# Optimization experiments

Measured on AMD Instinct MI355X. Metric: run time of the kernel, lower is better.

## Reference

```python
import jax, jax.numpy as jnp
import numpy as np

NDIM, NINEQ, NEQ = 1024, 512, 256
EPS = 1e-4       # Q regularization (module's eps)
N_ITERS = 25     # fixed primal-dual interior-point iterations
SIGMA = 0.1      # centering parameter


def setup_inputs() -> dict:
    key = jax.random.key(0)
    ks = jax.random.split(key, 5)
    L = jnp.tril(jax.random.uniform(ks[0], (NDIM, NDIM)))                      # tril(rand) as in torch init
    q = jax.random.uniform(ks[1], (NDIM,), minval=-1.0, maxval=1.0)
    G = jax.random.uniform(ks[2], (NINEQ, NDIM), minval=-1.0, maxval=1.0)
    A = jax.random.uniform(ks[3], (NEQ, NDIM), minval=-1.0, maxval=1.0)
    b = jax.random.uniform(ks[4], (NEQ,), minval=-1.0, maxval=1.0)
    x0 = jnp.zeros((NDIM,), jnp.float32)   # nn.Parameter(torch.zeros(ndim))
    s0 = jnp.ones((NINEQ,), jnp.float32)   # nn.Parameter(torch.ones(nineq))
    return {"L": L, "q": q, "G": G, "A": A, "b": b, "x0": x0, "s0": s0}


def _frac_to_boundary(v, dv):
    # max step alpha in (0,1] keeping v + alpha*dv > 0, with 0.99 backoff
    safe_dv = jnp.where(dv < 0, dv, -1.0)
    ratio = jnp.where(dv < 0, -v / safe_dv, 1.0)
    return jnp.min(ratio)


def _solve_qp(Q, q, G, h, A, b):
    n, m, p = q.shape[0], h.shape[0], b.shape[0]

    def step(state, _):
        x, s, z, y = state
        r_x = Q @ x + q + G.T @ z + A.T @ y          # dual residual
        r_p = G @ x + s - h                           # primal ineq residual
        r_y = A @ x - b                               # primal eq residual
        mu = jnp.dot(s, z) / m
        r_c = s * z - SIGMA * mu                      # centered complementarity
        D = z / s                                     # diag scaling
        H = Q + G.T @ (D[:, None] * G)                # reduced Hessian [n,n]
        KKT = jnp.block([[H, A.T], [A, jnp.zeros((p, p), Q.dtype)]])
        rhs = jnp.concatenate([-(r_x + G.T @ ((-r_c + z * r_p) / s)), -r_y])
        sol = jnp.linalg.solve(KKT, rhs)
        dx, dy = sol[:n], sol[n:]
        ds = -r_p - G @ dx
        dz = (-r_c - z * ds) / s
        alpha = 0.99 * jnp.minimum(1.0, jnp.minimum(_frac_to_boundary(s, ds), _frac_to_boundary(z, dz)))
        return (x + alpha * dx, s + alpha * ds, z + alpha * dz, y + alpha * dy), None

    init = (jnp.zeros((n,), Q.dtype), jnp.ones((m,), Q.dtype), jnp.ones((m,), Q.dtype), jnp.zeros((p,), Q.dtype))
    (x, s, z, y), _ = jax.lax.scan(step, init, None, length=N_ITERS)
    return x


def reference(L, q, G, A, b, x0, s0):
    Lt = jnp.tril(L)  # M * L with M = tril(ones)
    Q = Lt @ Lt.T + EPS * jnp.eye(L.shape[0], dtype=L.dtype)
    h = G @ x0 + s0   # learn_h branch (source's self.z0 is self.x0)
    return _solve_qp(Q, q, G, h, A, b)
```

## Files before the change

kernel.cpp:

```cpp
#include <hip/hip_runtime.h>
#include <hip/hip_bf16.h>


constexpr int ND = 1024;
constexpr int MI = 512;
constexpr int PE = 256;
constexpr int NM = 512;
constexpr int LDM = 520;
constexpr double EPSQ = 1e-4;
constexpr double SIG = 0.1;
constexpr int NITER = 25;

__device__ __forceinline__ double wred(double v) {
#pragma unroll
  for (int off = 32; off; off >>= 1) v += __shfl_down(v, off, 64);
  return v;
}

__global__ void k_prep(const float* __restrict__ Gf, const float* __restrict__ Af,
                       const float* __restrict__ qf, const float* __restrict__ bf,
                       float* __restrict__ GTf, float* __restrict__ ATf,
                       double* __restrict__ qd, double* __restrict__ bd,
                       double* __restrict__ xv, double* __restrict__ sv,
                       double* __restrict__ zv, double* __restrict__ yv,
                       double* __restrict__ scal) {
  if (blockIdx.x == 0 && threadIdx.x == 0) { scal[0] = 1.0; scal[1] = 0.0; }
  for (size_t idx = (size_t)blockIdx.x * blockDim.x + threadIdx.x;
       idx < (size_t)MI * ND; idx += (size_t)gridDim.x * blockDim.x) {
    int k = (int)(idx >> 10), i = (int)(idx & 1023);
    GTf[(size_t)i * MI + k] = Gf[idx];
    if (idx < (size_t)PE * ND) ATf[(size_t)i * PE + k] = Af[idx];
    if (idx < ND) { qd[idx] = (double)qf[idx]; xv[idx] = 0.0; }
    if (idx < MI) { sv[idx] = 1.0; zv[idx] = 1.0; }
    if (idx < PE) { bd[idx] = (double)bf[idx]; yv[idx] = 0.0; }
  }
}

__global__ __launch_bounds__(256) void k_h(const float* __restrict__ Gf,
                                           const float* __restrict__ x0f,
                                           const float* __restrict__ s0f,
                                           double* __restrict__ hd) {
  int wid = blockIdx.x * 4 + (int)(threadIdx.x >> 6), lane = threadIdx.x & 63;
  if (wid >= MI) return;
  double acc = 0;
  for (int c = lane; c < ND; c += 64) acc += (double)Gf[(size_t)wid * ND + c] * (double)x0f[c];
  acc = wred(acc);
  if (lane == 0) hd[wid] = acc + (double)s0f[wid];
}

__global__ __launch_bounds__(256) void k_qbuild(const float* __restrict__ Lf,
                                                double* __restrict__ Qd, double* __restrict__ LQ) {
  __shared__ double As[32][33], Bs[32][33];
  int i0 = blockIdx.y * 32, j0 = blockIdx.x * 32;
  int tx = threadIdx.x & 15, ty = threadIdx.x >> 4;
  double acc[2][2] = {};
  int kmax = (i0 < j0 ? i0 : j0) + 32;
  for (int k0 = 0; k0 < kmax; k0 += 32) {
    for (int l = threadIdx.x; l < 1024; l += 256) {
      int r = l >> 5, c = l & 31;
      As[r][c] = (k0 + c <= i0 + r) ? (double)Lf[(size_t)(i0 + r) * ND + k0 + c] : 0.0;
      Bs[r][c] = (k0 + c <= j0 + r) ? (double)Lf[(size_t)(j0 + r) * ND + k0 + c] : 0.0;
    }
    __syncthreads();
#pragma unroll
    for (int k = 0; k < 32; k++) {
      double a0 = As[2 * ty][k], a1 = As[2 * ty + 1][k];
      double b0 = Bs[2 * tx][k], b1 = Bs[2 * tx + 1][k];
      acc[0][0] += a0 * b0; acc[0][1] += a0 * b1;
      acc[1][0] += a1 * b0; acc[1][1] += a1 * b1;
    }
    __syncthreads();
  }
  for (int da = 0; da < 2; da++)
    for (int db = 0; db < 2; db++) {
      int i = i0 + 2 * ty + da, j = j0 + 2 * tx + db;
      double v = acc[da][db] + (i == j ? EPSQ : 0.0);
      Qd[(size_t)i * ND + j] = v;
      LQ[(size_t)i * ND + j] = v;
    }
}

__global__ __launch_bounds__(256) void k_chol_diag_inv(double* __restrict__ A, int lda, int kb,
                                                       double* __restrict__ DG) {
  __shared__ double a[64][65];
  __shared__ double invp[2080];
  __shared__ double dfloor;
  int t = threadIdx.x;
  size_t base = (size_t)kb * 64;
  for (int l = t; l < 4096; l += 256) { int r = l >> 6, c = l & 63; a[r][c] = A[(base + r) * lda + base + c]; }
  __syncthreads();
  if (t == 0) {
    double m = 0;
    for (int i = 0; i < 64; i++) m = fmax(m, fabs(a[i][i]));
    dfloor = m * 1e-28 + 1e-280;
  }
  __syncthreads();
  for (int j = 0; j < 64; j++) {
    if (t == 0) a[j][j] = sqrt(fmax(a[j][j], dfloor));
    __syncthreads();
    double piv = a[j][j];
    for (int r = j + 1 + t; r < 64; r += 256) a[r][j] /= piv;
    __syncthreads();
    int w = 63 - j;
    for (int l = t; l < w * w; l += 256) {
      int rr = j + 1 + l / w, cc = j + 1 + l % w;
      if (cc <= rr) a[rr][cc] -= a[rr][j] * a[cc][j];
    }
    __syncthreads();
  }
  for (int l = t; l < 4096; l += 256) { int r = l >> 6, c = l & 63; if (c <= r) A[(base + r) * lda + base + c] = a[r][c]; }
  if (t < 64) {
    int c = t;
    for (int i = c; i < 64; i++) {
      double v = (i == c) ? 1.0 : 0.0;
      for (int k = c; k < i; k++) v -= a[i][k] * invp[k * (k + 1) / 2 + c];
      invp[i * (i + 1) / 2 + c] = v / a[i][i];
    }
  }
  __syncthreads();
  for (int l = t; l < 4096; l += 256) {
    int r = l >> 6, c = l & 63;
    DG[(size_t)kb * 4096 + (size_t)c * 64 + r] = (c <= r) ? invp[r * (r + 1) / 2 + c] : 0.0;
  }
}

__global__ __launch_bounds__(256) void k_diag2(double* __restrict__ A, int lda, int kb,
                                               double* __restrict__ DG) {
  __shared__ double sh[6400];
  int t = threadIdx.x;
  if (blockIdx.x == 0) {
    double* a = sh;
    double* invp = sh + 4160;
    size_t base = (size_t)kb * 64;
    for (int l = t; l < 4096; l += 256) { int r = l >> 6, c = l & 63; a[r * 65 + c] = A[(base + r) * lda + base + c]; }
    __syncthreads();
    if (t == 0) {
      double m = 0;
      for (int i = 0; i < 64; i++) m = fmax(m, fabs(a[i * 65 + i]));
      sh[6272] = m * 1e-28 + 1e-280;
    }
    __syncthreads();
    double dfloor = sh[6272];
    for (int j = 0; j < 64; j++) {
      if (t == 0) a[j * 65 + j] = sqrt(fmax(a[j * 65 + j], dfloor));
      __syncthreads();
      double piv = a[j * 65 + j];
      for (int r = j + 1 + t; r < 64; r += 256) a[r * 65 + j] /= piv;
      __syncthreads();
      int w = 63 - j;
      for (int l = t; l < w * w; l += 256) {
        int rr = j + 1 + l / w, cc = j + 1 + l % w;
        if (cc <= rr) a[rr * 65 + cc] -= a[rr * 65 + j] * a[cc * 65 + j];
      }
      __syncthreads();
    }
    for (int l = t; l < 4096; l += 256) { int r = l >> 6, c = l & 63; if (c <= r) A[(base + r) * lda + base + c] = a[r * 65 + c]; }
    if (t < 64) {
      int c = t;
      for (int i = c; i < 64; i++) {
        double v = (i == c) ? 1.0 : 0.0;
        for (int k = c; k < i; k++) v -= a[i * 65 + k] * invp[k * (k + 1) / 2 + c];
        invp[i * (i + 1) / 2 + c] = v / a[i * 65 + i];
      }
    }
    __syncthreads();
    for (int l = t; l < 4096; l += 256) {
      int r = l >> 6, c = l & 63;
      DG[(size_t)kb * 4096 + (size_t)c * 64 + r] = (c <= r) ? invp[r * (r + 1) / 2 + c] : 0.0;
    }
  } else if (kb > 0) {
    int kbp = kb - 1;
    double* DT = sh;
    double* gseg = sh + 4096;
    double* pseg = sh + 4160;
    for (int l = t; l < 4096; l += 256) DT[l] = DG[(size_t)kbp * 4096 + l];
    if (t < 64) gseg[t] = A[(size_t)NM * lda + kbp * 64 + t];
    __syncthreads();
    if (t < 64) {
      double s = 0;
#pragma unroll
      for (int k = 0; k < 64; k++) s += gseg[k] * DT[k * 64 + t];
      pseg[t] = s;
    }
    __syncthreads();
    for (int c = kb * 64 + t; c < NM; c += 256) {
      double s = 0;
#pragma unroll
      for (int k = 0; k < 64; k++) s += pseg[k] * A[(size_t)c * lda + kbp * 64 + k];
      A[(size_t)NM * lda + c] -= s;
    }
    if (t < 64) A[(size_t)NM * lda + kbp * 64 + t] = pseg[t];
  }
}

__global__ __launch_bounds__(256) void k_chol_panel(double* __restrict__ A, int lda, int kb,
                                                    const double* __restrict__ DG) {
  __shared__ double B32[32][65];
  __shared__ double DT[64][64];
  int t = threadIdx.x;
  int r0 = (kb + 1) * 64 + blockIdx.x * 64;
  int c0 = kb * 64;
  for (int l = t; l < 4096; l += 256) DT[l >> 6][l & 63] = DG[(size_t)kb * 4096 + l];
  int wave = t >> 6, lane = t & 63;
  for (int h = 0; h < 2; ++h) {
    __syncthreads();
    for (int l = t; l < 2048; l += 256) { int r = l >> 6, c = l & 63; B32[r][c] = A[(size_t)(r0 + h * 32 + r) * lda + c0 + c]; }
    __syncthreads();
    for (int rr = 0; rr < 8; rr++) {
      int rl = wave * 8 + rr;
      double acc = 0;
#pragma unroll
      for (int c = 0; c < 64; c++) acc += B32[rl][c] * DT[c][lane];
      A[(size_t)(r0 + h * 32 + rl) * lda + c0 + lane] = acc;
    }
  }
}

__global__ __launch_bounds__(256) void k_chol_syrk(double* __restrict__ A, int lda, int kb) {
  int start = (kb + 1) * 64;
  int i0 = start + blockIdx.y * 32, j0 = start + blockIdx.x * 32;
  if (j0 > i0) return;
  __shared__ double As[32][33], Bs[32][33];
  int tx = threadIdx.x & 15, ty = threadIdx.x >> 4;
  double acc[2][2] = {};
  for (int k0 = 0; k0 < 64; k0 += 32) {
    for (int l = threadIdx.x; l < 1024; l += 256) {
      int r = l >> 5, c = l & 31;
      As[r][c] = A[(size_t)(i0 + r) * lda + kb * 64 + k0 + c];
      Bs[r][c] = A[(size_t)(j0 + r) * lda + kb * 64 + k0 + c];
    }
    __syncthreads();
#pragma unroll
    for (int k = 0; k < 32; k++) {
      double a0 = As[2 * ty][k], a1 = As[2 * ty + 1][k];
      double b0 = Bs[2 * tx][k], b1 = Bs[2 * tx + 1][k];
      acc[0][0] += a0 * b0; acc[0][1] += a0 * b1;
      acc[1][0] += a1 * b0; acc[1][1] += a1 * b1;
    }
    __syncthreads();
  }
  for (int da = 0; da < 2; da++)
    for (int db = 0; db < 2; db++) {
      int i = i0 + 2 * ty + da, j = j0 + 2 * tx + db;
      if (j <= i) A[(size_t)i * lda + j] -= acc[da][db];
    }
}

__global__ __launch_bounds__(256) void k_trsmf_g(const double* __restrict__ Lm, int lda,
                                                 double* __restrict__ X, int ldx,
                                                 const double* __restrict__ DG, int kb) {
  __shared__ double Lb[64][64];
  __shared__ double Xs[64][33];
  int t = threadIdx.x;
  int c0 = blockIdx.x * 32;
  int lane2 = t & 31, rbase = t >> 5;
  int row0 = kb * 64;
  double acc[8];
#pragma unroll
  for (int e = 0; e < 8; e++) acc[e] = (row0 + rbase + 8 * e == c0 + lane2) ? 1.0 : 0.0;
  for (int jb = 0; jb < kb; jb++) {
    for (int l = t; l < 4096; l += 256) { int r = l >> 6, c = l & 63; Lb[r][c] = Lm[(size_t)(row0 + r) * lda + jb * 64 + c]; }
    for (int l = t; l < 2048; l += 256) { int k = l >> 5, c = l & 31; Xs[k][c] = X[(size_t)(jb * 64 + k) * ldx + c0 + c]; }
    __syncthreads();
#pragma unroll 4
    for (int k = 0; k < 64; k++) {
      double wv = Xs[k][lane2];
#pragma unroll
      for (int e = 0; e < 8; e++) acc[e] -= Lb[rbase + 8 * e][k] * wv;
    }
    __syncthreads();
  }
  __syncthreads();
#pragma unroll
  for (int e = 0; e < 8; e++) Xs[rbase + 8 * e][lane2] = acc[e];
  for (int l = t; l < 4096; l += 256) Lb[l >> 6][l & 63] = DG[(size_t)kb * 4096 + l];
  __syncthreads();
#pragma unroll
  for (int e = 0; e < 8; e++) {
    int i = rbase + 8 * e;
    double s = 0;
#pragma unroll 4
    for (int k = 0; k < 64; k++) s += Lb[k][i] * Xs[k][lane2];
    X[(size_t)(row0 + i) * ldx + c0 + lane2] = s;
  }
}

__global__ __launch_bounds__(256) void k_trsmb_g(const double* __restrict__ Lm, int lda,
                                                 double* __restrict__ X, int ldx,
                                                 const double* __restrict__ DG, int kb, int nkb) {
  __shared__ double Lb[64][64];
  __shared__ double Xs[64][33];
  int t = threadIdx.x;
  int c0 = blockIdx.x * 32;
  int lane2 = t & 31, rbase = t >> 5;
  int row0 = kb * 64;
  double acc[8];
#pragma unroll
  for (int e = 0; e < 8; e++) acc[e] = X[(size_t)(row0 + rbase + 8 * e) * ldx + c0 + lane2];
  for (int jb = kb + 1; jb < nkb; jb++) {
    for (int l = t; l < 4096; l += 256) { int r = l >> 6, c = l & 63; Lb[r][c] = Lm[(size_t)(jb * 64 + r) * lda + kb * 64 + c]; }
    for (int l = t; l < 2048; l += 256) { int k = l >> 5, c = l & 31; Xs[k][c] = X[(size_t)(jb * 64 + k) * ldx + c0 + c]; }
    __syncthreads();
#pragma unroll 4
    for (int k = 0; k < 64; k++) {
      double wv = Xs[k][lane2];
#pragma unroll
      for (int e = 0; e < 8; e++) acc[e] -= Lb[k][rbase + 8 * e] * wv;
    }
    __syncthreads();
  }
  __syncthreads();
#pragma unroll
  for (int e = 0; e < 8; e++) Xs[rbase + 8 * e][lane2] = acc[e];
  for (int l = t; l < 4096; l += 256) Lb[l >> 6][l & 63] = DG[(size_t)kb * 4096 + l];
  __syncthreads();
#pragma unroll
  for (int e = 0; e < 8; e++) {
    int i = rbase + 8 * e;
    double s = 0;
#pragma unroll 4
    for (int k = 0; k < 64; k++) s += Lb[i][k] * Xs[k][lane2];
    X[(size_t)(row0 + i) * ldx + c0 + lane2] = s;
  }
}

__global__ __launch_bounds__(256) void k_aqi(const float* __restrict__ Af, const double* __restrict__ Qi,
                                             double* __restrict__ AQi) {
  __shared__ double As[32][33], Bs[32][33];
  int i0 = blockIdx.x * 32, a0 = blockIdx.y * 32;
  int tx = threadIdx.x & 15, ty = threadIdx.x >> 4;
  double acc[2][2] = {};
  for (int k0 = 0; k0 < ND; k0 += 32) {
    for (int l = threadIdx.x; l < 1024; l += 256) {
      int r = l >> 5, c = l & 31;
      As[r][c] = (double)Af[(size_t)(a0 + r) * ND + k0 + c];
      Bs[r][c] = Qi[(size_t)(k0 + r) * ND + i0 + c];
    }
    __syncthreads();
#pragma unroll
    for (int k = 0; k < 32; k++) {
      double a0v = As[2 * ty][k], a1v = As[2 * ty + 1][k];
      double b0v = Bs[k][2 * tx], b1v = Bs[k][2 * tx + 1];
      acc[0][0] += a0v * b0v; acc[0][1] += a0v * b1v;
      acc[1][0] += a1v * b0v; acc[1][1] += a1v * b1v;
    }
    __syncthreads();
  }
  for (int da = 0; da < 2; da++)
    for (int db = 0; db < 2; db++)
      AQi[(size_t)(a0 + 2 * ty + da) * ND + i0 + 2 * tx + db] = acc[da][db];
}

__global__ __launch_bounds__(256) void k_sa(const double* __restrict__ AQi, const float* __restrict__ Af,
                                            double* __restrict__ SA) {
  __shared__ double As[32][33], Bs[32][33];
  int a0 = blockIdx.y * 32, b0 = blockIdx.x * 32;
  int tx = threadIdx.x & 15, ty = threadIdx.x >> 4;
  double acc[2][2] = {};
  for (int k0 = 0; k0 < ND; k0 += 32) {
    for (int l = threadIdx.x; l < 1024; l += 256) {
      int r = l >> 5, c = l & 31;
      As[r][c] = AQi[(size_t)(a0 + r) * ND + k0 + c];
      Bs[r][c] = (double)Af[(size_t)(b0 + r) * ND + k0 + c];
    }
    __syncthreads();
#pragma unroll
    for (int k = 0; k < 32; k++) {
      double a0v = As[2 * ty][k], a1v = As[2 * ty + 1][k];
      double b0v = Bs[2 * tx][k], b1v = Bs[2 * tx + 1][k];
      acc[0][0] += a0v * b0v; acc[0][1] += a0v * b1v;
      acc[1][0] += a1v * b0v; acc[1][1] += a1v * b1v;
    }
    __syncthreads();
  }
  for (int da = 0; da < 2; da++)
    for (int db = 0; db < 2; db++)
      SA[(size_t)(a0 + 2 * ty + da) * PE + b0 + 2 * tx + db] = acc[da][db];
}

__global__ __launch_bounds__(256) void k_xy(const double* __restrict__ AQi, const double* __restrict__ SAi,
                                            double* __restrict__ XY) {
  __shared__ double As[32][33], Bs[32][33];
  int b0 = blockIdx.x * 32, i0 = blockIdx.y * 32;
  int tx = threadIdx.x & 15, ty = threadIdx.x >> 4;
  double acc[2][2] = {};
  for (int k0 = 0; k0 < PE; k0 += 32) {
    for (int l = threadIdx.x; l < 1024; l += 256) {
      int r = l >> 5, c = l & 31;
      As[r][c] = AQi[(size_t)(k0 + r) * ND + i0 + c];
      Bs[r][c] = SAi[(size_t)(k0 + r) * PE + b0 + c];
    }
    __syncthreads();
#pragma unroll
    for (int k = 0; k < 32; k++) {
      double a0v = As[k][2 * ty], a1v = As[k][2 * ty + 1];
      double b0v = Bs[k][2 * tx], b1v = Bs[k][2 * tx + 1];
      acc[0][0] += a0v * b0v; acc[0][1] += a0v * b1v;
      acc[1][0] += a1v * b0v; acc[1][1] += a1v * b1v;
    }
    __syncthreads();
  }
  for (int da = 0; da < 2; da++)
    for (int db = 0; db < 2; db++)
      XY[(size_t)(i0 + 2 * ty + da) * PE + b0 + 2 * tx + db] = acc[da][db];
}

__global__ __launch_bounds__(256) void k_xx(const double* __restrict__ Qi, const double* __restrict__ XY,
                                            const double* __restrict__ AQi, double* __restrict__ XX) {
  __shared__ double As[32][33], Bs[32][33];
  int j0 = blockIdx.x * 32, i0 = blockIdx.y * 32;
  int tx = threadIdx.x & 15, ty = threadIdx.x >> 4;
  double acc[2][2] = {};
  for (int k0 = 0; k0 < PE; k0 += 32) {
    for (int l = threadIdx.x; l < 1024; l += 256) {
      int r = l >> 5, c = l & 31;
      As[r][c] = XY[(size_t)(i0 + r) * PE + k0 + c];
      Bs[r][c] = AQi[(size_t)(k0 + r) * ND + j0 + c];
    }
    __syncthreads();
#pragma unroll
    for (int k = 0; k < 32; k++) {
      double a0v = As[2 * ty][k], a1v = As[2 * ty + 1][k];
      double b0v = Bs[k][2 * tx], b1v = Bs[k][2 * tx + 1];
      acc[0][0] += a0v * b0v; acc[0][1] += a0v * b1v;
      acc[1][0] += a1v * b0v; acc[1][1] += a1v * b1v;
    }
    __syncthreads();
  }
  for (int da = 0; da < 2; da++)
    for (int db = 0; db < 2; db++) {
      int i = i0 + 2 * ty + da, j = j0 + 2 * tx + db;
      XX[(size_t)i * ND + j] = Qi[(size_t)i * ND + j] - acc[da][db];
    }
}

__global__ __launch_bounds__(256) void k_fk0x(const float* __restrict__ Gf, const double* __restrict__ XX,
                                              double* __restrict__ FK0x) {
  __shared__ double As[32][33], Bs[32][33];
  int j0 = blockIdx.x * 32, g0 = blockIdx.y * 32;
  int tx = threadIdx.x & 15, ty = threadIdx.x >> 4;
  double acc[2][2] = {};
  for (int k0 = 0; k0 < ND; k0 += 32) {
    for (int l = threadIdx.x; l < 1024; l += 256) {
      int r = l >> 5, c = l & 31;
      As[r][c] = (double)Gf[(size_t)(g0 + r) * ND + k0 + c];
      Bs[r][c] = XX[(size_t)(k0 + r) * ND + j0 + c];
    }
    __syncthreads();
#pragma unroll
    for (int k = 0; k < 32; k++) {
      double a0v = As[2 * ty][k], a1v = As[2 * ty + 1][k];
      double b0v = Bs[k][2 * tx], b1v = Bs[k][2 * tx + 1];
      acc[0][0] += a0v * b0v; acc[0][1] += a0v * b1v;
      acc[1][0] += a1v * b0v; acc[1][1] += a1v * b1v;
    }
    __syncthreads();
  }
  for (int da = 0; da < 2; da++)
    for (int db = 0; db < 2; db++)
      FK0x[(size_t)(g0 + 2 * ty + da) * ND + j0 + 2 * tx + db] = acc[da][db];
}

__global__ __launch_bounds__(256) void k_fk0y(const float* __restrict__ Gf, const double* __restrict__ XY,
                                              double* __restrict__ FK0y) {
  __shared__ double As[32][33], Bs[32][33];
  int b0 = blockIdx.x * 32, g0 = blockIdx.y * 32;
  int tx = threadIdx.x & 15, ty = threadIdx.x >> 4;
  double acc[2][2] = {};
  for (int k0 = 0; k0 < ND; k0 += 32) {
    for (int l = threadIdx.x; l < 1024; l += 256) {
      int r = l >> 5, c = l & 31;
      As[r][c] = (double)Gf[(size_t)(g0 + r) * ND + k0 + c];
      Bs[r][c] = XY[(size_t)(k0 + r) * PE + b0 + c];
    }
    __syncthreads();
#pragma unroll
    for (int k = 0; k < 32; k++) {
      double a0v = As[2 * ty][k], a1v = As[2 * ty + 1][k];
      double b0v = Bs[k][2 * tx], b1v = Bs[k][2 * tx + 1];
      acc[0][0] += a0v * b0v; acc[0][1] += a0v * b1v;
      acc[1][0] += a1v * b0v; acc[1][1] += a1v * b1v;
    }
    __syncthreads();
  }
  for (int da = 0; da < 2; da++)
    for (int db = 0; db < 2; db++)
      FK0y[(size_t)(g0 + 2 * ty + da) * PE + b0 + 2 * tx + db] = acc[da][db];
}

__global__ __launch_bounds__(256) void k_smat(const double* __restrict__ FK0x, const float* __restrict__ Gf,
                                              double* __restrict__ S) {
  __shared__ double As[32][33], Bs[32][33];
  int g0 = blockIdx.y * 32, h0 = blockIdx.x * 32;
  int tx = threadIdx.x & 15, ty = threadIdx.x >> 4;
  double acc[2][2] = {};
  for (int k0 = 0; k0 < ND; k0 += 32) {
    for (int l = threadIdx.x; l < 1024; l += 256) {
      int r = l >> 5, c = l & 31;
      As[r][c] = FK0x[(size_t)(g0 + r) * ND + k0 + c];
      Bs[r][c] = (double)Gf[(size_t)(h0 + r) * ND + k0 + c];
    }
    __syncthreads();
#pragma unroll
    for (int k = 0; k < 32; k++) {
      double a0v = As[2 * ty][k], a1v = As[2 * ty + 1][k];
      double b0v = Bs[2 * tx][k], b1v = Bs[2 * tx + 1][k];
      acc[0][0] += a0v * b0v; acc[0][1] += a0v * b1v;
      acc[1][0] += a1v * b0v; acc[1][1] += a1v * b1v;
    }
    __syncthreads();
  }
  for (int da = 0; da < 2; da++)
    for (int db = 0; db < 2; db++)
      S[(size_t)(g0 + 2 * ty + da) * MI + h0 + 2 * tx + db] = acc[da][db];
}

__global__ __launch_bounds__(256) void k_tr(const double* __restrict__ src, double* __restrict__ dst,
                                            int R, int Cc) {
  __shared__ double tile[32][33];
  int r0 = blockIdx.y * 32, c0 = blockIdx.x * 32;
  for (int l = threadIdx.x; l < 1024; l += 256) {
    int r = l >> 5, c = l & 31;
    tile[r][c] = src[(size_t)(r0 + r) * Cc + c0 + c];
  }
  __syncthreads();
  for (int l = threadIdx.x; l < 1024; l += 256) {
    int r = l >> 5, c = l & 31;
    dst[(size_t)(c0 + r) * R + r0 + c] = tile[c][r];
  }
}

__global__ __launch_bounds__(256) void k_A1(const double* __restrict__ Qd, const float* __restrict__ Gf,
                                            const float* __restrict__ Af, const float* __restrict__ GTf,
                                            const float* __restrict__ ATf, const double* __restrict__ qd,
                                            const double* __restrict__ bd, const double* __restrict__ hd,
                                            const double* __restrict__ xv, const double* __restrict__ sv,
                                            const double* __restrict__ zv, const double* __restrict__ yv,
                                            const double* __restrict__ scal,
                                            double* __restrict__ rxv, double* __restrict__ rp,
                                            double* __restrict__ ry, double* __restrict__ uv,
                                            double* __restrict__ dinv) {
  int lane = threadIdx.x & 63;
  if (blockIdx.x < 256) {
    int wid = blockIdx.x * 4 + (int)(threadIdx.x >> 6);
    double acc = 0;
    for (int k = lane; k < ND; k += 64) acc += Qd[(size_t)wid * ND + k] * xv[k];
    for (int k = lane; k < MI; k += 64) acc += (double)GTf[(size_t)wid * MI + k] * zv[k];
    for (int k = lane; k < PE; k += 64) acc += (double)ATf[(size_t)wid * PE + k] * yv[k];
    acc = wred(acc);
    if (lane == 0) rxv[wid] = acc + qd[wid];
  } else {
    int wid = (blockIdx.x - 256) * 4 + (int)(threadIdx.x >> 6);
    if (wid < MI) {
      double acc = 0;
      for (int c = lane; c < ND; c += 64) acc += (double)Gf[(size_t)wid * ND + c] * xv[c];
      acc = wred(acc);
      if (lane == 0) {
        double s0 = sv[wid], z0 = zv[wid];
        double rpv = acc + s0 - hd[wid];
        rp[wid] = rpv;
        double rc0 = s0 * z0 - SIG * scal[0];
        uv[wid] = (-rc0 + z0 * rpv) / s0;
        dinv[wid] = s0 / z0;
      }
    } else {
      int r = wid - MI;
      double acc = 0;
      for (int c = lane; c < ND; c += 64) acc += (double)Af[(size_t)r * ND + c] * xv[c];
      acc = wred(acc);
      if (lane == 0) ry[r] = acc - bd[r];
    }
  }
}

__global__ __launch_bounds__(256) void k_A2(const double* __restrict__ rxv, const float* __restrict__ GTf,
                                            const double* __restrict__ uv, const double* __restrict__ dinv,
                                            const double* __restrict__ ry, const double* __restrict__ S,
                                            const double* __restrict__ FK0x, const double* __restrict__ FK0y,
                                            double* __restrict__ rhs1, double* __restrict__ Mm) {
  int t = threadIdx.x, lane = t & 63;
  if (blockIdx.x < 256) {
    int wid = blockIdx.x * 4 + (t >> 6);
    double acc = 0;
    for (int k = lane; k < MI; k += 64) acc += (double)GTf[(size_t)wid * MI + k] * uv[k];
    acc = wred(acc);
    if (lane == 0) rhs1[wid] = -(rxv[wid] + acc);
  } else if (blockIdx.x < 320) {
    int rbase = (blockIdx.x - 256) * 8;
    for (int rr = 0; rr < 8; ++rr) {
      int row = rbase + rr;
      for (int c = t; c < NM; c += 256) {
        double v = S[(size_t)row * MI + c];
        if (row == c) v += dinv[row];
        Mm[(size_t)row * LDM + c] = v;
      }
    }
  } else {
    int j = (blockIdx.x - 320) * 4 + (t >> 6);
    double acc = 0;
    for (int k = lane; k < ND; k += 64) acc += FK0x[(size_t)j * ND + k] * rxv[k];
    for (int m = lane; m < MI; m += 64) acc += S[(size_t)j * MI + m] * uv[m];
    for (int c = lane; c < PE; c += 64) acc += FK0y[(size_t)j * PE + c] * ry[c];
    acc = wred(acc);
    if (lane == 0) Mm[(size_t)NM * LDM + j] = -acc;
  }
}

__global__ __launch_bounds__(256) void k_bwd(const double* __restrict__ Mm, const double* __restrict__ DGC,
                                             double* __restrict__ solw) {
  __shared__ double DT[4096];
  __shared__ double gf[NM];
  __shared__ double acc4[4][64];
  __shared__ double tmp[64];
  int t = threadIdx.x;
  int i = t & 63, p4 = t >> 6;
  for (int l = t; l < NM; l += 256) gf[l] = Mm[(size_t)NM * LDM + l];
  for (int l = t; l < 4096; l += 256) DT[l] = DGC[(size_t)7 * 4096 + l];
  __syncthreads();
  if (t < 64) {
    double s = 0;
#pragma unroll
    for (int k = 0; k < 64; k++) s += gf[448 + k] * DT[k * 64 + t];
    tmp[t] = s;
  }
  __syncthreads();
  if (t < 64) gf[448 + t] = tmp[t];
  __syncthreads();
  for (int kb = 7; kb >= 0; --kb) {
    __syncthreads();
    for (int l = t; l < 4096; l += 256) DT[l] = DGC[(size_t)kb * 4096 + l];
    int tr0 = kb * 64 + 64;
    int R = NM - tr0;
    double s = 0;
    for (int rr = p4; rr < R; rr += 4)
      s += Mm[(size_t)(tr0 + rr) * LDM + kb * 64 + i] * gf[tr0 + rr];
    acc4[p4][i] = s;
    __syncthreads();
    if (t < 64) tmp[t] = gf[kb * 64 + t] - (acc4[0][t] + acc4[1][t] + acc4[2][t] + acc4[3][t]);
    __syncthreads();
    if (t < 64) {
      double v = 0;
#pragma unroll
      for (int l = 0; l < 64; l++) v += DT[t * 64 + l] * tmp[l];
      acc4[0][t] = v;
    }
    __syncthreads();
    if (t < 64) gf[kb * 64 + t] = acc4[0][t];
    __syncthreads();
  }
  for (int l = t; l < NM; l += 256) solw[l] = gf[l];
}

__global__ __launch_bounds__(512) void k_upd(const double* __restrict__ solw, const double* __restrict__ rp,
                                             const double* __restrict__ dinv, double* __restrict__ sv,
                                             double* __restrict__ zv, double* __restrict__ scal) {
  __shared__ double red[512];
  __shared__ double dsA[512];
  __shared__ double dzA[512];
  int t = threadIdx.x;
  double mu = scal[0];
  double s0 = sv[t], z0 = zv[t];
  double ds = -rp[t] - dinv[t] * solw[t];
  double rc0 = s0 * z0 - SIG * mu;
  double dz = (-rc0 - z0 * ds) / s0;
  dsA[t] = ds; dzA[t] = dz;
  double rs = (ds < 0.0) ? -s0 / ds : 1.0;
  double rz = (dz < 0.0) ? -z0 / dz : 1.0;
  red[t] = fmin(rs, rz);
  __syncthreads();
  for (int s2 = 256; s2; s2 >>= 1) { if (t < s2) red[t] = fmin(red[t], red[t + s2]); __syncthreads(); }
  double alpha = 0.99 * fmin(1.0, red[0]);
  if (!(alpha == alpha)) alpha = 0.0;
  double us = alpha * dsA[t], uz = alpha * dzA[t];
  if (isfinite(us)) sv[t] += us;
  if (isfinite(uz)) zv[t] += uz;
  __syncthreads();
  red[t] = sv[t] * zv[t];
  __syncthreads();
  for (int s2 = 256; s2; s2 >>= 1) { if (t < s2) red[t] += red[t + s2]; __syncthreads(); }
  if (t == 0) { scal[0] = red[0] / (double)MI; scal[1] = alpha; }
}

__global__ __launch_bounds__(256) void k_C(const double* __restrict__ XX, const double* __restrict__ XGT,
                                           const double* __restrict__ XY, const double* __restrict__ YXm,
                                           const double* __restrict__ YGT, const double* __restrict__ SAi,
                                           const double* __restrict__ rhs1, const double* __restrict__ solw,
                                           const double* __restrict__ ry, const double* __restrict__ scal,
                                           double* __restrict__ xv, double* __restrict__ yv) {
  int lane = threadIdx.x & 63;
  double al = scal[1];
  if (blockIdx.x < 256) {
    int wid = blockIdx.x * 4 + (int)(threadIdx.x >> 6);
    double acc = 0;
    for (int k = lane; k < ND; k += 64) acc += XX[(size_t)wid * ND + k] * rhs1[k];
    for (int m = lane; m < MI; m += 64) acc -= XGT[(size_t)wid * MI + m] * solw[m];
    for (int c = lane; c < PE; c += 64) acc -= XY[(size_t)wid * PE + c] * ry[c];
    acc = wred(acc);
    if (lane == 0) { double u = al * acc; if (isfinite(u)) xv[wid] += u; }
  } else {
    int r = (blockIdx.x - 256) * 4 + (int)(threadIdx.x >> 6);
    double acc = 0;
    for (int k = lane; k < ND; k += 64) acc += YXm[(size_t)r * ND + k] * rhs1[k];
    for (int m = lane; m < MI; m += 64) acc -= YGT[(size_t)r * MI + m] * solw[m];
    for (int c = lane; c < PE; c += 64) acc += SAi[(size_t)r * PE + c] * ry[c];
    acc = wred(acc);
    if (lane == 0) { double u = al * acc; if (isfinite(u)) yv[r] += u; }
  }
}

__global__ void k_out(const double* __restrict__ xv, float* __restrict__ out) {
  int i = blockIdx.x * blockDim.x + threadIdx.x;
  if (i < ND) out[i] = (float)xv[i];
}

__global__ void k_wsdiag(float mb, float* out) {
  int i = blockIdx.x * 256 + threadIdx.x;
  if (i < ND) out[i] = (i == 0 ? (65536.0f * (1.0f + mb)) : 0.0f);
}

extern "C" void kernel_launch(void* const* d_in, const int* in_sizes, int n_in,
                              void* d_out, int out_size, void* d_ws, size_t ws_size,
                              hipStream_t stream) {
  const float* Lf = (const float*)d_in[0];
  const float* qf = (const float*)d_in[1];
  const float* Gf = (const float*)d_in[2];
  const float* Af = (const float*)d_in[3];
  const float* bf = (const float*)d_in[4];
  const float* x0f = (const float*)d_in[5];
  const float* s0f = (const float*)d_in[6];

  double* w = (double*)d_ws;
  double* Qd  = w; w += (size_t)ND * ND;
  double* XX  = w; w += (size_t)ND * ND;
  double* R1  = w; w += (size_t)ND * ND;
  double* R2  = w; w += (size_t)ND * ND;
  double* XY  = w; w += (size_t)ND * PE;
  double* FK0xReg = w; w += (size_t)MI * ND;
  double* SA  = w; w += (size_t)PE * PE;
  double* DGH = w; w += (size_t)16 * 4096;
  double* DGA = w; w += (size_t)4 * 4096;
  double* DGC = w; w += (size_t)8 * 4096;
  double* qd = w; w += ND;  double* bd = w; w += PE;  double* hd = w; w += MI;
  double* xv = w; w += ND;  double* sv = w; w += MI;  double* zv = w; w += MI;  double* yv = w; w += PE;
  double* rxv = w; w += ND; double* rp = w; w += MI;  double* ry = w; w += PE;
  double* uv = w; w += MI;  double* dinv = w; w += MI;
  double* rhs1 = w; w += ND; double* solw = w; w += NM;
  double* scal = w; w += 16;
  float* GTf = (float*)w;
  float* ATf = GTf + (size_t)ND * MI;
  char* wend = (char*)(ATf + (size_t)ND * PE);
  size_t need = (size_t)(wend - (char*)d_ws);
  if (ws_size < need) {
    k_wsdiag<<<4, 256, 0, stream>>>((float)(ws_size >> 20), (float*)d_out);
    return;
  }

  double* Qi  = R1;
  double* XGT = R1;
  double* YXm = R1 + (size_t)ND * MI;
  double* YGT = R1 + (size_t)ND * MI + (size_t)PE * ND;
  double* LQ  = R2;
  double* Mm  = R2;
  double* FK0y = R2 + (size_t)(NM + 1) * LDM;
  double* SAi  = FK0y + (size_t)MI * PE;
  double* Smat = SAi + (size_t)PE * PE;
  double* AQi  = FK0xReg;
  double* FK0x = FK0xReg;

  k_prep<<<2048, 256, 0, stream>>>(Gf, Af, qf, bf, GTf, ATf, qd, bd, xv, sv, zv, yv, scal);
  k_h<<<128, 256, 0, stream>>>(Gf, x0f, s0f, hd);
  { dim3 g(32, 32); k_qbuild<<<g, 256, 0, stream>>>(Lf, Qd, LQ); }
  for (int kb = 0; kb < 16; kb++) {
    k_chol_diag_inv<<<1, 256, 0, stream>>>(LQ, ND, kb, DGH);
    int nb = 15 - kb;
    if (nb > 0) k_chol_panel<<<nb, 256, 0, stream>>>(LQ, ND, kb, DGH);
    int nt = 2 * nb;
    if (nt > 0) { dim3 gs(nt, nt); k_chol_syrk<<<gs, 256, 0, stream>>>(LQ, ND, kb); }
  }
  for (int kb = 0; kb < 16; kb++)  k_trsmf_g<<<32, 256, 0, stream>>>(LQ, ND, Qi, ND, DGH, kb);
  for (int kb = 15; kb >= 0; kb--) k_trsmb_g<<<32, 256, 0, stream>>>(LQ, ND, Qi, ND, DGH, kb, 16);
  { dim3 g(32, 8);  k_aqi<<<g, 256, 0, stream>>>(Af, Qi, AQi); }
  { dim3 g(8, 8);   k_sa<<<g, 256, 0, stream>>>(AQi, Af, SA); }
  for (int kb = 0; kb < 4; kb++) {
    k_chol_diag_inv<<<1, 256, 0, stream>>>(SA, PE, kb, DGA);
    int nb = 3 - kb;
    if (nb > 0) k_chol_panel<<<nb, 256, 0, stream>>>(SA, PE, kb, DGA);
    int nt = 2 * nb;
    if (nt > 0) { dim3 gs(nt, nt); k_chol_syrk<<<gs, 256, 0, stream>>>(SA, PE, kb); }
  }
  for (int kb = 0; kb < 4; kb++)  k_trsmf_g<<<8, 256, 0, stream>>>(SA, PE, SAi, PE, DGA, kb);
  for (int kb = 3; kb >= 0; kb--) k_trsmb_g<<<8, 256, 0, stream>>>(SA, PE, SAi, PE, DGA, kb, 4);
  { dim3 g(8, 32);  k_xy<<<g, 256, 0, stream>>>(AQi, SAi, XY); }
  { dim3 g(32, 32); k_xx<<<g, 256, 0, stream>>>(Qi, XY, AQi, XX); }
  { dim3 g(32, 16); k_fk0x<<<g, 256, 0, stream>>>(Gf, XX, FK0x); }
  { dim3 g(8, 16);  k_fk0y<<<g, 256, 0, stream>>>(Gf, XY, FK0y); }
  { dim3 g(16, 16); k_smat<<<g, 256, 0, stream>>>(FK0x, Gf, Smat); }
  { dim3 g(32, 16); k_tr<<<g, 256, 0, stream>>>(FK0x, XGT, MI, ND); }
  { dim3 g(8, 32);  k_tr<<<g, 256, 0, stream>>>(XY, YXm, ND, PE); }
  { dim3 g(8, 16);  k_tr<<<g, 256, 0, stream>>>(FK0y, YGT, MI, PE); }

  for (int it = 0; it < NITER; ++it) {
    k_A1<<<448, 256, 0, stream>>>(Qd, Gf, Af, GTf, ATf, qd, bd, hd, xv, sv, zv, yv, scal,
                                  rxv, rp, ry, uv, dinv);
    k_A2<<<448, 256, 0, stream>>>(rxv, GTf, uv, dinv, ry, Smat, FK0x, FK0y, rhs1, Mm);
    for (int kb = 0; kb < 8; kb++) {
      k_diag2<<<2, 256, 0, stream>>>(Mm, LDM, kb, DGC);
      int nb = 7 - kb;
      if (nb > 0) {
        k_chol_panel<<<nb, 256, 0, stream>>>(Mm, LDM, kb, DGC);
        dim3 gs(2 * nb, 2 * nb);
        k_chol_syrk<<<gs, 256, 0, stream>>>(Mm, LDM, kb);
      }
    }
    k_bwd<<<1, 256, 0, stream>>>(Mm, DGC, solw);
    k_upd<<<1, 512, 0, stream>>>(solw, rp, dinv, sv, zv, scal);
    k_C<<<320, 256, 0, stream>>>(XX, XGT, XY, YXm, YGT, SAi, rhs1, solw, ry, scal, xv, yv);
  }
  k_out<<<4, 256, 0, stream>>>(xv, (float*)d_out);
}
```

Before: 43.94 ms.

## Fuse Cholesky panel, SYRK and next diagonal factor into one kernel per step

Replaces the separate diag/panel/syrk launches of the blocked Cholesky with a single k_fps kernel per block column. Each block recomputes the panel product on the fly, writes panel results to a separate buffer, applies the trailing update, and factors the next diagonal block inside the same launch. The forward and backward triangular solves of the per-iteration KKT system are merged with the step update into one kernel. The aim is to cut kernel launches and serial dependencies. The cost is redundant panel GEMMs, large dynamic shared memory (about 130KB) and extra scratch buffers.

```diff
diff --git a/kernel.cpp b/kernel.cpp
--- a/kernel.cpp
+++ b/kernel.cpp
@@ -124,126 +124,147 @@
   }
 }
 
-__global__ __launch_bounds__(256) void k_diag2(double* __restrict__ A, int lda, int kb,
-                                               double* __restrict__ DG) {
-  __shared__ double sh[6400];
-  int t = threadIdx.x;
-  if (blockIdx.x == 0) {
-    double* a = sh;
-    double* invp = sh + 4160;
-    size_t base = (size_t)kb * 64;
-    for (int l = t; l < 4096; l += 256) { int r = l >> 6, c = l & 63; a[r * 65 + c] = A[(base + r) * lda + base + c]; }
-    __syncthreads();
-    if (t == 0) {
-      double m = 0;
-      for (int i = 0; i < 64; i++) m = fmax(m, fabs(a[i * 65 + i]));
-      sh[6272] = m * 1e-28 + 1e-280;
-    }
-    __syncthreads();
-    double dfloor = sh[6272];
-    for (int j = 0; j < 64; j++) {
-      if (t == 0) a[j * 65 + j] = sqrt(fmax(a[j * 65 + j], dfloor));
-      __syncthreads();
-      double piv = a[j * 65 + j];
-      for (int r = j + 1 + t; r < 64; r += 256) a[r * 65 + j] /= piv;
-      __syncthreads();
-      int w = 63 - j;
-      for (int l = t; l < w * w; l += 256) {
-        int rr = j + 1 + l / w, cc = j + 1 + l % w;
-        if (cc <= rr) a[rr * 65 + cc] -= a[rr * 65 + j] * a[cc * 65 + j];
-      }
-      __syncthreads();
-    }
-    for (int l = t; l < 4096; l += 256) { int r = l >> 6, c = l & 63; if (c <= r) A[(base + r) * lda + base + c] = a[r * 65 + c]; }
-    if (t < 64) {
-      int c = t;
-      for (int i = c; i < 64; i++) {
-        double v = (i == c) ? 1.0 : 0.0;
-        for (int k = c; k < i; k++) v -= a[i * 65 + k] * invp[k * (k + 1) / 2 + c];
-        invp[i * (i + 1) / 2 + c] = v / a[i * 65 + i];
-      }
-    }
-    __syncthreads();
+__global__ __launch_bounds__(256) void k_fps(double* __restrict__ A, int lda,
+                                             double* __restrict__ PL, int ldp,
+                                             double* __restrict__ DG, int kb) {
+  extern __shared__ double sh[];
+  double* DT = sh;
+  double* Bs = sh + 4096;
+  double* Pi = sh + 8256;
+  double* Pj = sh + 12416;
+  const int t = threadIdx.x;
+  int idx = blockIdx.x;
+  int bi = (int)((sqrtf(8.0f * (float)idx + 1.0f) - 1.0f) * 0.5f);
+  while ((bi + 1) * (bi + 2) / 2 <= idx) ++bi;
+  while (bi * (bi + 1) / 2 > idx) --bi;
+  int bj = idx - bi * (bi + 1) / 2;
+  const int ib = kb + 1 + bi, jb = kb + 1 + bj;
+  const int tx = t & 15, ty = t >> 4;
+
+  for (int l = t; l < 4096; l += 256) DT[l] = DG[(size_t)kb * 4096 + l];
+  for (int l = t; l < 4096; l += 256) { int r = l >> 6, c = l & 63; Bs[r * 65 + c] = A[(size_t)(ib * 64 + r) * lda + kb * 64 + c]; }
+  __syncthreads();
+  {
+    double acc[4][4] = {};
+    for (int k = 0; k < 64; ++k) {
+      double b0 = Bs[ty * 65 + k], b1 = Bs[(ty + 16) * 65 + k];
+      double b2 = Bs[(ty + 32) * 65 + k], b3 = Bs[(ty + 48) * 65 + k];
+      double d0 = DT[k * 64 + tx], d1 = DT[k * 64 + tx + 16];
+      double d2 = DT[k * 64 + tx + 32], d3 = DT[k * 64 + tx + 48];
+      acc[0][0] += b0 * d0; acc[0][1] += b0 * d1; acc[0][2] += b0 * d2; acc[0][3] += b0 * d3;
+      acc[1][0] += b1 * d0; acc[1][1] += b1 * d1; acc[1][2] += b1 * d2; acc[1][3] += b1 * d3;
+      acc[2][0] += b2 * d0; acc[2][1] += b2 * d1; acc[2][2] += b2 * d2; acc[2][3] += b2 * d3;
+      acc[3][0] += b3 * d0; acc[3][1] += b3 * d1; acc[3][2] += b3 * d2; acc[3][3] += b3 * d3;
+    }
+    __syncthreads();
+    for (int e = 0; e < 4; ++e)
+      for (int f = 0; f < 4; ++f) Pi[(ty + 16 * e) * 65 + tx + 16 * f] = acc[e][f];
+  }
+  __syncthreads();
+  if (ib == jb) {
     for (int l = t; l < 4096; l += 256) {
       int r = l >> 6, c = l & 63;
-      DG[(size_t)kb * 4096 + (size_t)c * 64 + r] = (c <= r) ? invp[r * (r + 1) / 2 + c] : 0.0;
-    }
-  } else if (kb > 0) {
-    int kbp = kb - 1;
-    double* DT = sh;
-    double* gseg = sh + 4096;
-    double* pseg = sh + 4160;
-    for (int l = t; l < 4096; l += 256) DT[l] = DG[(size_t)kbp * 4096 + l];
-    if (t < 64) gseg[t] = A[(size_t)NM * lda + kbp * 64 + t];
-    __syncthreads();
-    if (t < 64) {
-      double s = 0;
-#pragma unroll
-      for (int k = 0; k < 64; k++) s += gseg[k] * DT[k * 64 + t];
-      pseg[t] = s;
-    }
-    __syncthreads();
-    for (int c = kb * 64 + t; c < NM; c += 256) {
-      double s = 0;
-#pragma unroll
-      for (int k = 0; k < 64; k++) s += pseg[k] * A[(size_t)c * lda + kbp * 64 + k];
-      A[(size_t)NM * lda + c] -= s;
-    }
-    if (t < 64) A[(size_t)NM * lda + kbp * 64 + t] = pseg[t];
-  }
-}
-
-__global__ __launch_bounds__(256) void k_chol_panel(double* __restrict__ A, int lda, int kb,
-                                                    const double* __restrict__ DG) {
-  __shared__ double B32[32][65];
-  __shared__ double DT[64][64];
-  int t = threadIdx.x;
-  int r0 = (kb + 1) * 64 + blockIdx.x * 64;
-  int c0 = kb * 64;
-  for (int l = t; l < 4096; l += 256) DT[l >> 6][l & 63] = DG[(size_t)kb * 4096 + l];
-  int wave = t >> 6, lane = t & 63;
-  for (int h = 0; h < 2; ++h) {
-    __syncthreads();
-    for (int l = t; l < 2048; l += 256) { int r = l >> 6, c = l & 63; B32[r][c] = A[(size_t)(r0 + h * 32 + r) * lda + c0 + c]; }
-    __syncthreads();
-    for (int rr = 0; rr < 8; rr++) {
-      int rl = wave * 8 + rr;
-      double acc = 0;
-#pragma unroll
-      for (int c = 0; c < 64; c++) acc += B32[rl][c] * DT[c][lane];
-      A[(size_t)(r0 + h * 32 + rl) * lda + c0 + lane] = acc;
-    }
-  }
-}
-
-__global__ __launch_bounds__(256) void k_chol_syrk(double* __restrict__ A, int lda, int kb) {
-  int start = (kb + 1) * 64;
-  int i0 = start + blockIdx.y * 32, j0 = start + blockIdx.x * 32;
-  if (j0 > i0) return;
-  __shared__ double As[32][33], Bs[32][33];
-  int tx = threadIdx.x & 15, ty = threadIdx.x >> 4;
-  double acc[2][2] = {};
-  for (int k0 = 0; k0 < 64; k0 += 32) {
-    for (int l = threadIdx.x; l < 1024; l += 256) {
-      int r = l >> 5, c = l & 31;
-      As[r][c] = A[(size_t)(i0 + r) * lda + kb * 64 + k0 + c];
-      Bs[r][c] = A[(size_t)(j0 + r) * lda + kb * 64 + k0 + c];
-    }
-    __syncthreads();
-#pragma unroll
-    for (int k = 0; k < 32; k++) {
-      double a0 = As[2 * ty][k], a1 = As[2 * ty + 1][k];
-      double b0 = Bs[2 * tx][k], b1 = Bs[2 * tx + 1][k];
-      acc[0][0] += a0 * b0; acc[0][1] += a0 * b1;
-      acc[1][0] += a1 * b0; acc[1][1] += a1 * b1;
-    }
-    __syncthreads();
-  }
-  for (int da = 0; da < 2; da++)
-    for (int db = 0; db < 2; db++) {
-      int i = i0 + 2 * ty + da, j = j0 + 2 * tx + db;
-      if (j <= i) A[(size_t)i * lda + j] -= acc[da][db];
-    }
+      PL[(size_t)(ib * 64 + r) * ldp + kb * 64 + c] = Pi[r * 65 + c];
+    }
+    double* a = Pj;
+    {
+      double acc[4][4] = {};
+      for (int k = 0; k < 64; ++k) {
+        double p0 = Pi[ty * 65 + k], p1 = Pi[(ty + 16) * 65 + k];
+        double p2 = Pi[(ty + 32) * 65 + k], p3 = Pi[(ty + 48) * 65 + k];
+        double q0 = Pi[tx * 65 + k], q1 = Pi[(tx + 16) * 65 + k];
+        double q2 = Pi[(tx + 32) * 65 + k], q3 = Pi[(tx + 48) * 65 + k];
+        acc[0][0] += p0 * q0; acc[0][1] += p0 * q1; acc[0][2] += p0 * q2; acc[0][3] += p0 * q3;
+        acc[1][0] += p1 * q0; acc[1][1] += p1 * q1; acc[1][2] += p1 * q2; acc[1][3] += p1 * q3;
+        acc[2][0] += p2 * q0; acc[2][1] += p2 * q1; acc[2][2] += p2 * q2; acc[2][3] += p2 * q3;
+        acc[3][0] += p3 * q0; acc[3][1] += p3 * q1; acc[3][2] += p3 * q2; acc[3][3] += p3 * q3;
+      }
+      for (int e = 0; e < 4; ++e)
+        for (int f = 0; f < 4; ++f) {
+          int r = ty + 16 * e, c = tx + 16 * f;
+          a[r * 65 + c] = A[(size_t)(ib * 64 + r) * lda + jb * 64 + c] - acc[e][f];
+        }
+    }
+    __syncthreads();
+    if (ib == kb + 1) {
+      if (t == 0) {
+        double m = 0;
+        for (int i = 0; i < 64; i++) m = fmax(m, fabs(a[i * 65 + i]));
+        sh[16576] = m * 1e-28 + 1e-280;
+      }
+      __syncthreads();
+      double dfloor = sh[16576];
+      for (int j = 0; j < 64; ++j) {
+        if (t == 0) a[j * 65 + j] = sqrt(fmax(a[j * 65 + j], dfloor));
+        __syncthreads();
+        double piv = a[j * 65 + j];
+        for (int r = j + 1 + t; r < 64; r += 256) a[r * 65 + j] /= piv;
+        __syncthreads();
+        int w = 63 - j;
+        for (int l = t; l < w * w; l += 256) {
+          int rr = j + 1 + l / w, cc = j + 1 + l % w;
+          if (cc <= rr) a[rr * 65 + cc] -= a[rr * 65 + j] * a[cc * 65 + j];
+        }
+        __syncthreads();
+      }
+      double* invp = Bs;
+      if (t < 64) {
+        int c = t;
+        for (int i = c; i < 64; ++i) {
+          double v = (i == c) ? 1.0 : 0.0;
+          for (int k = c; k < i; ++k) v -= a[i * 65 + k] * invp[k * (k + 1) / 2 + c];
+          invp[i * (i + 1) / 2 + c] = v / a[i * 65 + i];
+        }
+      }
+      __syncthreads();
+      for (int l = t; l < 4096; l += 256) {
+        int r = l >> 6, c = l & 63;
+        DG[(size_t)(kb + 1) * 4096 + (size_t)c * 64 + r] = (c <= r) ? invp[r * (r + 1) / 2 + c] : 0.0;
+      }
+    } else {
+      for (int l = t; l < 4096; l += 256) {
+        int r = l >> 6, c = l & 63;
+        A[(size_t)(ib * 64 + r) * lda + jb * 64 + c] = a[r * 65 + c];
+      }
+    }
+  } else {
+    for (int l = t; l < 4096; l += 256) { int r = l >> 6, c = l & 63; Bs[r * 65 + c] = A[(size_t)(jb * 64 + r) * lda + kb * 64 + c]; }
+    __syncthreads();
+    {
+      double acc[4][4] = {};
+      for (int k = 0; k < 64; ++k) {
+        double b0 = Bs[ty * 65 + k], b1 = Bs[(ty + 16) * 65 + k];
+        double b2 = Bs[(ty + 32) * 65 + k], b3 = Bs[(ty + 48) * 65 + k];
+        double d0 = DT[k * 64 + tx], d1 = DT[k * 64 + tx + 16];
+        double d2 = DT[k * 64 + tx + 32], d3 = DT[k * 64 + tx + 48];
+        acc[0][0] += b0 * d0; acc[0][1] += b0 * d1; acc[0][2] += b0 * d2; acc[0][3] += b0 * d3;
+        acc[1][0] += b1 * d0; acc[1][1] += b1 * d1; acc[1][2] += b1 * d2; acc[1][3] += b1 * d3;
+        acc[2][0] += b2 * d0; acc[2][1] += b2 * d1; acc[2][2] += b2 * d2; acc[2][3] += b2 * d3;
+        acc[3][0] += b3 * d0; acc[3][1] += b3 * d1; acc[3][2] += b3 * d2; acc[3][3] += b3 * d3;
+      }
+      __syncthreads();
+      for (int e = 0; e < 4; ++e)
+        for (int f = 0; f < 4; ++f) Pj[(ty + 16 * e) * 65 + tx + 16 * f] = acc[e][f];
+    }
+    __syncthreads();
+    double acc[4][4] = {};
+    for (int k = 0; k < 64; ++k) {
+      double p0 = Pi[ty * 65 + k], p1 = Pi[(ty + 16) * 65 + k];
+      double p2 = Pi[(ty + 32) * 65 + k], p3 = Pi[(ty + 48) * 65 + k];
+      double q0 = Pj[tx * 65 + k], q1 = Pj[(tx + 16) * 65 + k];
+      double q2 = Pj[(tx + 32) * 65 + k], q3 = Pj[(tx + 48) * 65 + k];
+      acc[0][0] += p0 * q0; acc[0][1] += p0 * q1; acc[0][2] += p0 * q2; acc[0][3] += p0 * q3;
+      acc[1][0] += p1 * q0; acc[1][1] += p1 * q1; acc[1][2] += p1 * q2; acc[1][3] += p1 * q3;
+      acc[2][0] += p2 * q0; acc[2][1] += p2 * q1; acc[2][2] += p2 * q2; acc[2][3] += p2 * q3;
+      acc[3][0] += p3 * q0; acc[3][1] += p3 * q1; acc[3][2] += p3 * q2; acc[3][3] += p3 * q3;
+    }
+    for (int e = 0; e < 4; ++e)
+      for (int f = 0; f < 4; ++f) {
+        int r = ty + 16 * e, c = tx + 16 * f;
+        size_t off = (size_t)(ib * 64 + r) * lda + jb * 64 + c;
+        A[off] -= acc[e][f];
+      }
+  }
 }
 
 __global__ __launch_bounds__(256) void k_trsmf_g(const double* __restrict__ Lm, int lda,
@@ -606,61 +627,72 @@
   }
 }
 
-__global__ __launch_bounds__(256) void k_bwd(const double* __restrict__ Mm, const double* __restrict__ DGC,
-                                             double* __restrict__ solw) {
+__global__ __launch_bounds__(512) void k_bwdupd(const double* __restrict__ Mm, const double* __restrict__ PL,
+                                                const double* __restrict__ DGC, const double* __restrict__ rp,
+                                                const double* __restrict__ dinv, double* __restrict__ sv,
+                                                double* __restrict__ zv, double* __restrict__ scal,
+                                                double* __restrict__ solw) {
   __shared__ double DT[4096];
-  __shared__ double gf[NM];
-  __shared__ double acc4[4][64];
+  __shared__ double g[NM];
+  __shared__ double pseg[64];
+  __shared__ double acc8[8][64];
   __shared__ double tmp[64];
-  int t = threadIdx.x;
-  int i = t & 63, p4 = t >> 6;
-  for (int l = t; l < NM; l += 256) gf[l] = Mm[(size_t)NM * LDM + l];
-  for (int l = t; l < 4096; l += 256) DT[l] = DGC[(size_t)7 * 4096 + l];
-  __syncthreads();
-  if (t < 64) {
-    double s = 0;
-#pragma unroll
-    for (int k = 0; k < 64; k++) s += gf[448 + k] * DT[k * 64 + t];
-    tmp[t] = s;
-  }
-  __syncthreads();
-  if (t < 64) gf[448 + t] = tmp[t];
-  __syncthreads();
-  for (int kb = 7; kb >= 0; --kb) {
-    __syncthreads();
-    for (int l = t; l < 4096; l += 256) DT[l] = DGC[(size_t)kb * 4096 + l];
-    int tr0 = kb * 64 + 64;
-    int R = NM - tr0;
-    double s = 0;
-    for (int rr = p4; rr < R; rr += 4)
-      s += Mm[(size_t)(tr0 + rr) * LDM + kb * 64 + i] * gf[tr0 + rr];
-    acc4[p4][i] = s;
-    __syncthreads();
-    if (t < 64) tmp[t] = gf[kb * 64 + t] - (acc4[0][t] + acc4[1][t] + acc4[2][t] + acc4[3][t]);
-    __syncthreads();
-    if (t < 64) {
-      double v = 0;
-#pragma unroll
-      for (int l = 0; l < 64; l++) v += DT[t * 64 + l] * tmp[l];
-      acc4[0][t] = v;
-    }
-    __syncthreads();
-    if (t < 64) gf[kb * 64 + t] = acc4[0][t];
-    __syncthreads();
-  }
-  for (int l = t; l < NM; l += 256) solw[l] = gf[l];
-}
-
-__global__ __launch_bounds__(512) void k_upd(const double* __restrict__ solw, const double* __restrict__ rp,
-                                             const double* __restrict__ dinv, double* __restrict__ sv,
-                                             double* __restrict__ zv, double* __restrict__ scal) {
   __shared__ double red[512];
   __shared__ double dsA[512];
   __shared__ double dzA[512];
   int t = threadIdx.x;
+  for (int l = t; l < NM; l += 512) g[l] = Mm[(size_t)NM * LDM + l];
+  for (int kbp = 0; kbp < 8; ++kbp) {
+    __syncthreads();
+    for (int l = t; l < 4096; l += 512) DT[l] = DGC[(size_t)kbp * 4096 + l];
+    __syncthreads();
+    if (t < 64) {
+      double s = 0;
+#pragma unroll
+      for (int k = 0; k < 64; k++) s += g[kbp * 64 + k] * DT[k * 64 + t];
+      pseg[t] = s;
+    }
+    __syncthreads();
+    for (int c = (kbp + 1) * 64 + t; c < NM; c += 512) {
+      double s = 0;
+#pragma unroll
+      for (int k = 0; k < 64; k++) s += pseg[k] * PL[(size_t)c * NM + kbp * 64 + k];
+      g[c] -= s;
+    }
+    if (t < 64) g[kbp * 64 + t] = pseg[t];
+  }
+  int i8 = t & 63, p8 = t >> 6;
+  for (int kb = 7; kb >= 0; --kb) {
+    __syncthreads();
+    for (int l = t; l < 4096; l += 512) DT[l] = DGC[(size_t)kb * 4096 + l];
+    __syncthreads();
+    int tr0 = kb * 64 + 64;
+    double s = 0;
+    for (int rr = p8; rr < NM - tr0; rr += 8)
+      s += PL[(size_t)(tr0 + rr) * NM + kb * 64 + i8] * g[tr0 + rr];
+    acc8[p8][i8] = s;
+    __syncthreads();
+    if (t < 64) {
+      double v = g[kb * 64 + t];
+#pragma unroll
+      for (int p = 0; p < 8; p++) v -= acc8[p][t];
+      tmp[t] = v;
+    }
+    __syncthreads();
+    if (t < 64) {
+      double v = 0;
+#pragma unroll
+      for (int l = 0; l < 64; l++) v += DT[t * 64 + l] * tmp[l];
+      pseg[t] = v;
+    }
+    __syncthreads();
+    if (t < 64) g[kb * 64 + t] = pseg[t];
+  }
+  __syncthreads();
+  solw[t] = g[t];
   double mu = scal[0];
   double s0 = sv[t], z0 = zv[t];
-  double ds = -rp[t] - dinv[t] * solw[t];
+  double ds = -rp[t] - dinv[t] * g[t];
   double rc0 = s0 * z0 - SIG * mu;
   double dz = (-rc0 - z0 * ds) / s0;
   dsA[t] = ds; dzA[t] = dz;
@@ -737,6 +769,7 @@
   double* XY  = w; w += (size_t)ND * PE;
   double* FK0xReg = w; w += (size_t)MI * ND;
   double* SA  = w; w += (size_t)PE * PE;
+  double* PLi = w; w += (size_t)NM * NM;
   double* DGH = w; w += (size_t)16 * 4096;
   double* DGA = w; w += (size_t)4 * 4096;
   double* DGC = w; w += (size_t)8 * 4096;
@@ -766,30 +799,30 @@
   double* Smat = SAi + (size_t)PE * PE;
   double* AQi  = FK0xReg;
   double* FK0x = FK0xReg;
+  double* PLQ  = XX;
+  double* PLA  = XY;
+
+  const size_t ldsFPS = (size_t)16640 * sizeof(double);
 
   k_prep<<<2048, 256, 0, stream>>>(Gf, Af, qf, bf, GTf, ATf, qd, bd, xv, sv, zv, yv, scal);
   k_h<<<128, 256, 0, stream>>>(Gf, x0f, s0f, hd);
   { dim3 g(32, 32); k_qbuild<<<g, 256, 0, stream>>>(Lf, Qd, LQ); }
-  for (int kb = 0; kb < 16; kb++) {
-    k_chol_diag_inv<<<1, 256, 0, stream>>>(LQ, ND, kb, DGH);
-    int nb = 15 - kb;
-    if (nb > 0) k_chol_panel<<<nb, 256, 0, stream>>>(LQ, ND, kb, DGH);
-    int nt = 2 * nb;
-    if (nt > 0) { dim3 gs(nt, nt); k_chol_syrk<<<gs, 256, 0, stream>>>(LQ, ND, kb); }
-  }
-  for (int kb = 0; kb < 16; kb++)  k_trsmf_g<<<32, 256, 0, stream>>>(LQ, ND, Qi, ND, DGH, kb);
-  for (int kb = 15; kb >= 0; kb--) k_trsmb_g<<<32, 256, 0, stream>>>(LQ, ND, Qi, ND, DGH, kb, 16);
+  k_chol_diag_inv<<<1, 256, 0, stream>>>(LQ, ND, 0, DGH);
+  for (int kb = 0; kb < 15; kb++) {
+    int nt = 15 - kb;
+    k_fps<<<nt * (nt + 1) / 2, 256, ldsFPS, stream>>>(LQ, ND, PLQ, ND, DGH, kb);
+  }
+  for (int kb = 0; kb < 16; kb++)  k_trsmf_g<<<32, 256, 0, stream>>>(PLQ, ND, Qi, ND, DGH, kb);
+  for (int kb = 15; kb >= 0; kb--) k_trsmb_g<<<32, 256, 0, stream>>>(PLQ, ND, Qi, ND, DGH, kb, 16);
   { dim3 g(32, 8);  k_aqi<<<g, 256, 0, stream>>>(Af, Qi, AQi); }
   { dim3 g(8, 8);   k_sa<<<g, 256, 0, stream>>>(AQi, Af, SA); }
-  for (int kb = 0; kb < 4; kb++) {
-    k_chol_diag_inv<<<1, 256, 0, stream>>>(SA, PE, kb, DGA);
-    int nb = 3 - kb;
-    if (nb > 0) k_chol_panel<<<nb, 256, 0, stream>>>(SA, PE, kb, DGA);
-    int nt = 2 * nb;
-    if (nt > 0) { dim3 gs(nt, nt); k_chol_syrk<<<gs, 256, 0, stream>>>(SA, PE, kb); }
-  }
-  for (int kb = 0; kb < 4; kb++)  k_trsmf_g<<<8, 256, 0, stream>>>(SA, PE, SAi, PE, DGA, kb);
-  for (int kb = 3; kb >= 0; kb--) k_trsmb_g<<<8, 256, 0, stream>>>(SA, PE, SAi, PE, DGA, kb, 4);
+  k_chol_diag_inv<<<1, 256, 0, stream>>>(SA, PE, 0, DGA);
+  for (int kb = 0; kb < 3; kb++) {
+    int nt = 3 - kb;
+    k_fps<<<nt * (nt + 1) / 2, 256, ldsFPS, stream>>>(SA, PE, PLA, PE, DGA, kb);
+  }
+  for (int kb = 0; kb < 4; kb++)  k_trsmf_g<<<8, 256, 0, stream>>>(PLA, PE, SAi, PE, DGA, kb);
+  for (int kb = 3; kb >= 0; kb--) k_trsmb_g<<<8, 256, 0, stream>>>(PLA, PE, SAi, PE, DGA, kb, 4);
   { dim3 g(8, 32);  k_xy<<<g, 256, 0, stream>>>(AQi, SAi, XY); }
   { dim3 g(32, 32); k_xx<<<g, 256, 0, stream>>>(Qi, XY, AQi, XX); }
   { dim3 g(32, 16); k_fk0x<<<g, 256, 0, stream>>>(Gf, XX, FK0x); }
@@ -803,17 +836,12 @@
     k_A1<<<448, 256, 0, stream>>>(Qd, Gf, Af, GTf, ATf, qd, bd, hd, xv, sv, zv, yv, scal,
                                   rxv, rp, ry, uv, dinv);
     k_A2<<<448, 256, 0, stream>>>(rxv, GTf, uv, dinv, ry, Smat, FK0x, FK0y, rhs1, Mm);
-    for (int kb = 0; kb < 8; kb++) {
-      k_diag2<<<2, 256, 0, stream>>>(Mm, LDM, kb, DGC);
-      int nb = 7 - kb;
-      if (nb > 0) {
-        k_chol_panel<<<nb, 256, 0, stream>>>(Mm, LDM, kb, DGC);
-        dim3 gs(2 * nb, 2 * nb);
-        k_chol_syrk<<<gs, 256, 0, stream>>>(Mm, LDM, kb);
-      }
-    }
-    k_bwd<<<1, 256, 0, stream>>>(Mm, DGC, solw);
-    k_upd<<<1, 512, 0, stream>>>(solw, rp, dinv, sv, zv, scal);
+    k_chol_diag_inv<<<1, 256, 0, stream>>>(Mm, LDM, 0, DGC);
+    for (int kb = 0; kb < 7; kb++) {
+      int nt = 7 - kb;
+      k_fps<<<nt * (nt + 1) / 2, 256, ldsFPS, stream>>>(Mm, LDM, PLi, NM, DGC, kb);
+    }
+    k_bwdupd<<<1, 512, 0, stream>>>(Mm, PLi, DGC, rp, dinv, sv, zv, scal, solw);
     k_C<<<320, 256, 0, stream>>>(XX, XGT, XY, YXm, YGT, SAi, rhs1, solw, ry, scal, xv, yv);
   }
   k_out<<<4, 256, 0, stream>>>(xv, (float*)d_out);
```

New measurement: 39.16 ms. -10.9%, faster.
